# Kernel tuning notes

Hardware: AMD Instinct MI355X
Metric: run time of the kernel (lower is better)

The kernel has to match this reference:

```python
import jax, jax.numpy as jnp
import numpy as np

D1 = 512
D2 = 1024  # = 2*D1 (concat of x1,y1 along channels)
B, S = 4, 2048


def _self_attn(x, Wq, bq, Wk, bk, Wv, bv):
    # Linear layers use torch convention: out = x @ W.T + b
    q = jnp.einsum('bsd,ed->bse', x, Wq) + bq
    k = jnp.einsum('bsd,ed->bse', x, Wk) + bk
    v = jnp.einsum('bsd,ed->bse', x, Wv) + bv
    # NOTE: original module has no 1/sqrt(d) scaling — keep it faithful.
    scores = jnp.einsum('bqe,bke->bqk', q, k)  # [B,S,S]
    attn = jax.nn.softmax(scores, axis=-1)
    return jnp.einsum('bqk,bke->bqe', attn, v)


def setup_inputs() -> dict:
    key = jax.random.key(0)
    ks = jax.random.split(key, 18)
    s1 = 1.0 / np.sqrt(D1)
    s2 = 1.0 / np.sqrt(D2)
    return {
        'x': jax.random.normal(ks[0], (B, S, D1), jnp.float32),
        'y': jax.random.normal(ks[1], (B, S, D1), jnp.float32),
        'sa1_Wq': jax.random.normal(ks[2], (D1, D1), jnp.float32) * s1,
        'sa1_bq': jnp.zeros((D1,), jnp.float32),
        'sa1_Wk': jax.random.normal(ks[3], (D1, D1), jnp.float32) * s1,
        'sa1_bk': jnp.zeros((D1,), jnp.float32),
        'sa1_Wv': jax.random.normal(ks[4], (D1, D1), jnp.float32) * s1,
        'sa1_bv': jnp.zeros((D1,), jnp.float32),
        'sa2_Wq': jax.random.normal(ks[5], (D2, D2), jnp.float32) * s2,
        'sa2_bq': jnp.zeros((D2,), jnp.float32),
        'sa2_Wk': jax.random.normal(ks[6], (D2, D2), jnp.float32) * s2,
        'sa2_bk': jnp.zeros((D2,), jnp.float32),
        'sa2_Wv': jax.random.normal(ks[7], (D2, D2), jnp.float32) * s2,
        'sa2_bv': jnp.zeros((D2,), jnp.float32),
        'weight1': jnp.ones((1,), jnp.float32),
        'weight2': jnp.ones((1,), jnp.float32),
    }


def reference(x, y, sa1_Wq, sa1_bq, sa1_Wk, sa1_bk, sa1_Wv, sa1_bv,
              sa2_Wq, sa2_bq, sa2_Wk, sa2_bk, sa2_Wv, sa2_bv,
              weight1, weight2):
    x1 = _self_attn(x, sa1_Wq, sa1_bq, sa1_Wk, sa1_bk, sa1_Wv, sa1_bv)
    x1 = x1 + y * weight2
    y1 = _self_attn(y, sa1_Wq, sa1_bq, sa1_Wk, sa1_bk, sa1_Wv, sa1_bv)
    y1 = y1 + x * weight1
    temp = jnp.concatenate((x1, y1), axis=2)  # [B,S,2*D1]
    return _self_attn(temp, sa2_Wq, sa2_bq, sa2_Wk, sa2_bk, sa2_Wv, sa2_bv)
```

## Files before the change

kernel.cpp:

```cpp
#include <hip/hip_runtime.h>
#include <hip/hip_bf16.h>
#include <cstdint>
#include <cstddef>


typedef __bf16 bf16;
typedef __attribute__((ext_vector_type(8))) __bf16 bf16x8;
typedef __attribute__((ext_vector_type(4))) __bf16 bf16x4;
typedef __attribute__((ext_vector_type(4))) float f32x4;

__device__ __forceinline__ void gld16(const bf16* g, bf16* s) {
    __builtin_amdgcn_global_load_lds(
        (const __attribute__((address_space(1))) void*)g,
        (__attribute__((address_space(3))) void*)s, 16, 0, 0);
}

#define WAIT_VM8   __builtin_amdgcn_s_waitcnt(8 | (7 << 4) | (0xF << 8))
#define WAIT_VM0   __builtin_amdgcn_s_waitcnt(0 | (7 << 4) | (0xF << 8))
#define WAIT_LGKM0 __builtin_amdgcn_s_waitcnt(0xF | (7 << 4) | (0 << 8) | (3 << 14))

__device__ __forceinline__ int swz(int row, int g) {
    return row * 64 + ((g ^ (row & 7)) << 3);
}

__global__ __launch_bounds__(256) void gemm_split(
    const bf16* __restrict__ A, long lda, long psA, long bsA,
    const bf16* __restrict__ B, long ldb, long psB, long bsB,
    void* __restrict__ C, long ldc, long psC, long bsC, int mode,
    const float* __restrict__ bias, const float* __restrict__ bias2, int nsplit,
    const float* __restrict__ resid, long ldr, long bsR,
    const float* __restrict__ scale,
    int K, int split, int nx, int ny, int nz)
{
    __shared__ __align__(16) bf16 As[2][128 * 64];
    __shared__ __align__(16) bf16 Bs[2][128 * 64];

    const int t    = threadIdx.x;
    const int wave = t >> 6;
    const int lane = t & 63;
    const int wr   = wave >> 1;
    const int wc   = wave & 1;
    const int r16  = lane & 15;
    const int quad = lane >> 4;

    const int g    = blockIdx.x;
    const int xcd  = g & 7;
    const int tk   = g >> 3;
    const int nst8 = gridDim.x >> 7;
    const int st   = xcd * nst8 + (tk >> 4);
    const int p    = tk & 15;
    const int snx  = nx >> 2, sny = ny >> 2;
    const int spz  = snx * sny;
    const int zz   = st / spz;
    const int rS   = st - zz * spz;
    const int sy   = rS / snx;
    const int sx   = rS - sy * snx;
    const int yb   = sy * 4 + (p >> 2);
    const int xb   = sx * 4 + (p & 3);

    const int  kh   = zz / nz;
    const long z    = zz - (long)kh * nz;
    const long kOff = (long)kh * K;

    const long row0 = (long)yb * 128;
    const long col0 = (long)xb * 128;

    const int srow = (lane >> 3);
    const int scol = ((lane & 7) ^ srow) * 8;

    const int ktiles = K >> 6;
    const int T = split * ktiles;

    const bf16* Az = A + z * bsA;
    const bf16* Bz = B + z * bsB;

    auto prefetch = [&](int ti, int buf) {
        const int ph = ti / ktiles;
        const int kt = (ti - ph * ktiles) << 6;
        const bf16* Ab = Az + (ph == 1 ? psA : 0);
        const bf16* Bb = Bz + (ph == 2 ? psB : 0);
#pragma unroll
        for (int p2 = 0; p2 < 4; ++p2) {
            const int chunk = wave * 32 + p2 * 8;
            gld16(Ab + (row0 + chunk + srow) * lda + kt + kOff + scol, &As[buf][chunk * 64]);
            gld16(Bb + (col0 + chunk + srow) * ldb + kt + kOff + scol, &Bs[buf][chunk * 64]);
        }
    };

    f32x4 acc[4][4];
#pragma unroll
    for (int r = 0; r < 4; ++r)
#pragma unroll
        for (int c = 0; c < 4; ++c)
            acc[r][c] = (f32x4){0.f, 0.f, 0.f, 0.f};

    prefetch(0, 0);
    prefetch(1, 1);
    for (int ti = 0; ti < T; ++ti) {
        const int cur = ti & 1;
        if (ti + 1 < T) WAIT_VM8; else WAIT_VM0;
        __builtin_amdgcn_s_barrier();
        bf16x8 af[2][4], bg[2][4];
#pragma unroll
        for (int kk = 0; kk < 2; ++kk) {
            const int g0 = (kk << 2) + quad;
#pragma unroll
            for (int r = 0; r < 4; ++r)
                af[kk][r] = *reinterpret_cast<const bf16x8*>(&As[cur][swz(wr * 64 + r * 16 + r16, g0)]);
#pragma unroll
            for (int c = 0; c < 4; ++c)
                bg[kk][c] = *reinterpret_cast<const bf16x8*>(&Bs[cur][swz(wc * 64 + c * 16 + r16, g0)]);
        }
        WAIT_LGKM0;
        __builtin_amdgcn_s_barrier();
        if (ti + 2 < T) prefetch(ti + 2, cur);
#pragma unroll
        for (int kk = 0; kk < 2; ++kk)
#pragma unroll
            for (int r = 0; r < 4; ++r)
#pragma unroll
                for (int c = 0; c < 4; ++c)
                    acc[r][c] = __builtin_amdgcn_mfma_f32_16x16x32_bf16(af[kk][r], bg[kk][c], acc[r][c], 0, 0, 0);
    }

    const float scv = resid ? *scale : 0.f;

#pragma unroll
    for (int r = 0; r < 4; ++r) {
#pragma unroll
        for (int c = 0; c < 4; ++c) {
            long gcol = col0 + wc * 64 + c * 16 + r16;
            float bv = 0.f;
            if (bias) bv = (gcol < nsplit) ? bias[gcol] : bias2[gcol - nsplit];
#pragma unroll
            for (int i = 0; i < 4; ++i) {
                long grow = row0 + wr * 64 + r * 16 + quad * 4 + i;
                float val = acc[r][c][i] + bv;
                if (mode == 0) {
                    if (resid) val += resid[z * bsR + grow * ldr + gcol] * scv;
                    ((float*)C)[z * bsC + grow * ldc + gcol] = val;
                } else if (mode == 1) {
                    if (resid) val += resid[z * bsR + grow * ldr + gcol] * scv;
                    bf16* Cb = (bf16*)C + z * bsC;
                    bf16 h = (bf16)val;
                    Cb[grow * ldc + gcol] = h;
                    Cb[psC + grow * ldc + gcol] = (bf16)(val - (float)h);
                } else if (mode == 3) {
                    ((float*)C)[(long)kh * psC + z * bsC + grow * ldc + gcol] = val;
                } else {
                    long b = grow >> 11, s = grow & 2047;
                    bf16* Cb = (bf16*)C + b * bsC;
                    bf16 h = (bf16)val;
                    Cb[gcol * ldc + s] = h;
                    Cb[psC + gcol * ldc + s] = (bf16)(val - (float)h);
                }
            }
        }
    }
}

__global__ __launch_bounds__(512) void gemm256(
    const bf16* __restrict__ A, long lda, long psA, long bsA,
    const bf16* __restrict__ B, long ldb, long psB, long bsB,
    void* __restrict__ C, long ldc, long psC, long bsC, int mode,
    const float* __restrict__ bias, const float* __restrict__ bias2, int nsplit,
    int K, int split, int nx, int ny)
{
    __shared__ __align__(16) bf16 As[2][256 * 64];
    __shared__ __align__(16) bf16 Bs[2][256 * 64];

    const int t    = threadIdx.x;
    const int wave = t >> 6;
    const int lane = t & 63;
    const int wm   = wave >> 2;
    const int wn   = wave & 3;
    const int r16  = lane & 15;
    const int quad = lane >> 4;

    const int g     = blockIdx.x;
    const int chunk = gridDim.x >> 3;
    const int idx   = (g & 7) * chunk + (g >> 3);
    const int tpz   = nx * ny;
    const int z     = idx / tpz;
    const int r0i   = idx - z * tpz;
    const int ty    = r0i / nx;
    const int tx    = r0i - ty * nx;
    const long row0 = (long)ty * 256;
    const long col0 = (long)tx * 256;

    const int srow = lane >> 3;
    const int scol = ((lane & 7) ^ srow) * 8;

    const int ktiles = K >> 6;
    const int T = split * ktiles;

    const bf16* Az = A + (long)z * bsA;
    const bf16* Bz = B + (long)z * bsB;

    auto prefetch = [&](int ti, int buf) {
        const int ph = ti / ktiles;
        const int kt = (ti - ph * ktiles) << 6;
        const bf16* Ab = Az + (ph == 1 ? psA : 0);
        const bf16* Bb = Bz + (ph == 2 ? psB : 0);
#pragma unroll
        for (int p2 = 0; p2 < 4; ++p2) {
            const int chnk = wave * 32 + p2 * 8;
            gld16(Ab + (row0 + chnk + srow) * lda + kt + scol, &As[buf][chnk * 64]);
            gld16(Bb + (col0 + chnk + srow) * ldb + kt + scol, &Bs[buf][chnk * 64]);
        }
    };

    f32x4 acc[8][4];
#pragma unroll
    for (int r = 0; r < 8; ++r)
#pragma unroll
        for (int c = 0; c < 4; ++c)
            acc[r][c] = (f32x4){0.f, 0.f, 0.f, 0.f};

    prefetch(0, 0);
    prefetch(1, 1);
    for (int ti = 0; ti < T; ++ti) {
        const int cur = ti & 1;
        if (ti + 1 < T) WAIT_VM8; else WAIT_VM0;
        __builtin_amdgcn_s_barrier();

        bf16x8 afA[4][2], afB[4][2], bg[2][2][2];
#pragma unroll
        for (int kk = 0; kk < 2; ++kk) {
            const int g0 = (kk << 2) + quad;
#pragma unroll
            for (int r = 0; r < 4; ++r)
                afA[r][kk] = *reinterpret_cast<const bf16x8*>(
                    &As[cur][swz(wm * 128 + r * 16 + r16, g0)]);
        }
#pragma unroll
        for (int kk = 0; kk < 2; ++kk) {
            const int g0 = (kk << 2) + quad;
#pragma unroll
            for (int c = 0; c < 2; ++c)
                bg[0][c][kk] = *reinterpret_cast<const bf16x8*>(
                    &Bs[cur][swz(wn * 64 + c * 16 + r16, g0)]);
        }
#pragma unroll
        for (int kk = 0; kk < 2; ++kk) {
            const int g0 = (kk << 2) + quad;
#pragma unroll
            for (int c = 0; c < 2; ++c)
                bg[1][c][kk] = *reinterpret_cast<const bf16x8*>(
                    &Bs[cur][swz(wn * 64 + (2 + c) * 16 + r16, g0)]);
        }
#pragma unroll
        for (int kk = 0; kk < 2; ++kk) {
            const int g0 = (kk << 2) + quad;
#pragma unroll
            for (int r = 0; r < 4; ++r)
                afB[r][kk] = *reinterpret_cast<const bf16x8*>(
                    &As[cur][swz(wm * 128 + (4 + r) * 16 + r16, g0)]);
        }

        __builtin_amdgcn_s_setprio(1);
#pragma unroll
        for (int kk = 0; kk < 2; ++kk)
#pragma unroll
            for (int r = 0; r < 4; ++r)
#pragma unroll
                for (int c = 0; c < 2; ++c)
                    acc[r][c] = __builtin_amdgcn_mfma_f32_16x16x32_bf16(
                        afA[r][kk], bg[0][c][kk], acc[r][c], 0, 0, 0);
#pragma unroll
        for (int kk = 0; kk < 2; ++kk)
#pragma unroll
            for (int r = 0; r < 4; ++r)
#pragma unroll
                for (int c = 0; c < 2; ++c)
                    acc[r][2 + c] = __builtin_amdgcn_mfma_f32_16x16x32_bf16(
                        afA[r][kk], bg[1][c][kk], acc[r][2 + c], 0, 0, 0);
        __builtin_amdgcn_s_setprio(0);

        __builtin_amdgcn_sched_barrier(0);
        WAIT_LGKM0;
        __builtin_amdgcn_s_barrier();
        if (ti + 2 < T) prefetch(ti + 2, cur);

        __builtin_amdgcn_s_setprio(1);
#pragma unroll
        for (int kk = 0; kk < 2; ++kk)
#pragma unroll
            for (int r = 0; r < 4; ++r)
#pragma unroll
                for (int c = 0; c < 2; ++c)
                    acc[4 + r][c] = __builtin_amdgcn_mfma_f32_16x16x32_bf16(
                        afB[r][kk], bg[0][c][kk], acc[4 + r][c], 0, 0, 0);
#pragma unroll
        for (int kk = 0; kk < 2; ++kk)
#pragma unroll
            for (int r = 0; r < 4; ++r)
#pragma unroll
                for (int c = 0; c < 2; ++c)
                    acc[4 + r][2 + c] = __builtin_amdgcn_mfma_f32_16x16x32_bf16(
                        afB[r][kk], bg[1][c][kk], acc[4 + r][2 + c], 0, 0, 0);
        __builtin_amdgcn_s_setprio(0);
    }

#pragma unroll
    for (int r = 0; r < 8; ++r) {
#pragma unroll
        for (int c = 0; c < 4; ++c) {
            const long gcol = col0 + wn * 64 + c * 16 + r16;
            float bv = 0.f;
            if (bias) bv = (gcol < nsplit) ? bias[gcol] : bias2[gcol - nsplit];
#pragma unroll
            for (int i = 0; i < 4; ++i) {
                const long grow = row0 + wm * 128 + r * 16 + quad * 4 + i;
                float val = acc[r][c][i] + bv;
                if (mode == 0) {
                    ((float*)C)[(long)z * bsC + grow * ldc + gcol] = val;
                } else {
                    bf16* Cb = (bf16*)C + (long)z * bsC;
                    bf16 h = (bf16)val;
                    Cb[grow * ldc + gcol] = h;
                    Cb[psC + grow * ldc + gcol] = (bf16)(val - (float)h);
                }
            }
        }
    }
}

__global__ __launch_bounds__(256) void reduce_pv(
    const float* __restrict__ p0, const float* __restrict__ p1,
    const float* __restrict__ resid, const float* __restrict__ scale,
    bf16* __restrict__ outp, long psC)
{
    const long gid = (long)blockIdx.x * 256 + threadIdx.x;
    const long f4  = gid * 4;
    const long z   = f4 >> 20;
    const long rem = f4 & ((1L << 20) - 1);
    const long row = rem >> 9;
    const long col = rem & 511;
    const float scv = *scale;
    f32x4 a = *reinterpret_cast<const f32x4*>(p0 + f4);
    f32x4 b = *reinterpret_cast<const f32x4*>(p1 + f4);
    f32x4 r = *reinterpret_cast<const f32x4*>(resid + f4);
    bf16x4 h, l;
#pragma unroll
    for (int j = 0; j < 4; ++j) {
        float v = a[j] + b[j] + r[j] * scv;
        h[j] = (bf16)v;
        l[j] = (bf16)(v - (float)h[j]);
    }
    bf16* dst = outp + z * (2048L * 1024) + row * 1024 + col;
    *reinterpret_cast<bf16x4*>(dst) = h;
    *reinterpret_cast<bf16x4*>(dst + psC) = l;
}

__global__ __launch_bounds__(256) void softmax_planes(float* __restrict__ S)
{
    __shared__ float redm[4], reds[4];
    float* srow = S + (long)blockIdx.x * 2048;
    const int t = threadIdx.x;
    const int lane = t & 63;
    const int wave = t >> 6;

    f32x4 v0 = *reinterpret_cast<const f32x4*>(srow + t * 4);
    f32x4 v1 = *reinterpret_cast<const f32x4*>(srow + 1024 + t * 4);

    float m = v0[0];
#pragma unroll
    for (int i = 1; i < 4; ++i) m = fmaxf(m, v0[i]);
#pragma unroll
    for (int i = 0; i < 4; ++i) m = fmaxf(m, v1[i]);
#pragma unroll
    for (int off = 32; off > 0; off >>= 1) m = fmaxf(m, __shfl_xor(m, off));
    if (lane == 0) redm[wave] = m;
    __syncthreads();
    m = fmaxf(fmaxf(redm[0], redm[1]), fmaxf(redm[2], redm[3]));

    float s = 0.f;
#pragma unroll
    for (int i = 0; i < 4; ++i) { v0[i] = __expf(v0[i] - m); s += v0[i]; }
#pragma unroll
    for (int i = 0; i < 4; ++i) { v1[i] = __expf(v1[i] - m); s += v1[i]; }
#pragma unroll
    for (int off = 32; off > 0; off >>= 1) s += __shfl_xor(s, off);
    if (lane == 0) reds[wave] = s;
    __syncthreads();
    s = reds[0] + reds[1] + reds[2] + reds[3];
    float inv = 1.f / s;

    bf16x4 h0, h1, l0, l1;
#pragma unroll
    for (int i = 0; i < 4; ++i) {
        float a = v0[i] * inv, b = v1[i] * inv;
        h0[i] = (bf16)a; l0[i] = (bf16)(a - (float)h0[i]);
        h1[i] = (bf16)b; l1[i] = (bf16)(b - (float)h1[i]);
    }
    bf16* ph = (bf16*)srow;
    *reinterpret_cast<bf16x4*>(ph + t * 4) = h0;
    *reinterpret_cast<bf16x4*>(ph + 1024 + t * 4) = h1;
    *reinterpret_cast<bf16x4*>(ph + 2048 + t * 4) = l0;
    *reinterpret_cast<bf16x4*>(ph + 3072 + t * 4) = l1;
}

__global__ __launch_bounds__(256) void split2_f32(
    const float* __restrict__ in, bf16* __restrict__ hi, bf16* __restrict__ lo)
{
    long i = ((long)blockIdx.x * 256 + threadIdx.x) * 4;
    f32x4 v = *reinterpret_cast<const f32x4*>(in + i);
    bf16x4 h, l;
#pragma unroll
    for (int j = 0; j < 4; ++j) {
        h[j] = (bf16)v[j];
        l[j] = (bf16)(v[j] - (float)h[j]);
    }
    *reinterpret_cast<bf16x4*>(hi + i) = h;
    *reinterpret_cast<bf16x4*>(lo + i) = l;
}

extern "C" void kernel_launch(void* const* d_in, const int* in_sizes, int n_in,
                              void* d_out, int out_size, void* d_ws, size_t ws_size,
                              hipStream_t stream)
{
    const float* x   = (const float*)d_in[0];
    const float* y   = (const float*)d_in[1];
    const float* Wq1 = (const float*)d_in[2];
    const float* bq1 = (const float*)d_in[3];
    const float* Wk1 = (const float*)d_in[4];
    const float* bk1 = (const float*)d_in[5];
    const float* Wv1 = (const float*)d_in[6];
    const float* bv1 = (const float*)d_in[7];
    const float* Wq2 = (const float*)d_in[8];
    const float* bq2 = (const float*)d_in[9];
    const float* Wk2 = (const float*)d_in[10];
    const float* bk2 = (const float*)d_in[11];
    const float* Wv2 = (const float*)d_in[12];
    const float* bv2 = (const float*)d_in[13];
    const float* w1  = (const float*)d_in[14];
    const float* w2  = (const float*)d_in[15];
    float* out = (float*)d_out;

    const size_t MB = 1ull << 20;
    char* ws = (char*)d_ws;
    const long S = 2048, M4 = 8192, E1 = 512, E2 = 1024;
    const long W1ps = E1 * E1, W2ps = E2 * E2;

    const int cfg = (ws_size >= 207 * MB) ? 2 : 0;

    auto gemm = [&](const bf16* A, long lda, long psA, long bsA,
                    const bf16* B, long ldb, long psB, long bsB,
                    void* C, long ldc, long psC, long bsC, int mode,
                    const float* bias, const float* bias2, int nsplit,
                    const float* resid, long ldr, long bsR,
                    const float* scale, int M, int N, int K, int split,
                    int gz, int nz) {
        int nx = N / 128, ny = M / 128;
        dim3 g((unsigned)(nx * ny * gz));
        gemm_split<<<g, dim3(256), 0, stream>>>(
            A, lda, psA, bsA, B, ldb, psB, bsB, C, ldc, psC, bsC, mode,
            bias, bias2, nsplit, resid, ldr, bsR, scale, K, split, nx, ny, nz);
    };
    auto g256 = [&](const bf16* A, long lda, long psA, long bsA,
                    const bf16* B, long ldb, long psB, long bsB,
                    void* C, long ldc, long psC, long bsC, int mode,
                    const float* bias, const float* bias2, int nsplit,
                    int K, int split, int M, int N, int gz) {
        int nx = N / 256, ny = M / 256;
        gemm256<<<dim3((unsigned)(nx * ny * gz)), dim3(512), 0, stream>>>(
            A, lda, psA, bsA, B, ldb, psB, bsB, C, ldc, psC, bsC, mode,
            bias, bias2, nsplit, K, split, nx, ny);
    };
    auto conv2 = [&](const float* in, bf16* hi, bf16* lo, long n) {
        split2_f32<<<dim3((unsigned)(n / 1024)), dim3(256), 0, stream>>>(in, hi, lo);
    };

    if (cfg == 2) {
        bf16* xyp   = (bf16*)d_out;
        bf16* Wqk1p = (bf16*)(ws + 0 * MB);
        bf16* Wv1p  = (bf16*)(ws + 2 * MB);
        bf16* Wqk2p = (bf16*)(ws + 3 * MB);
        bf16* Wv2p  = (bf16*)(ws + 11 * MB);
        bf16* temp  = (bf16*)(ws + 15 * MB);
        bf16* qk    = (bf16*)(ws + 47 * MB);
        bf16* vt    = (bf16*)(ws + 111 * MB);
        float* Sc   = (float*)(ws + 143 * MB);

        const long PXY = 16384L * 512;
        const long PW1 = 1024L * 512;
        const long PW2 = 2048L * 1024;
        const long PQ1 = 16384L * 1024;
        const long PQ2 = 8192L * 2048;
        const long PT  = 8192L * 1024;
        const long BV1 = 2 * E1 * S;
        const long BV2 = 2 * E2 * S;
        const long PVH = 4L * 2048 * 512;
        float* pvScr = (float*)d_out;

        conv2(x, xyp, xyp + PXY, M4 * E1);
        conv2(y, xyp + M4 * E1, xyp + PXY + M4 * E1, M4 * E1);
        conv2(Wq1, Wqk1p, Wqk1p + PW1, W1ps);
        conv2(Wk1, Wqk1p + W1ps, Wqk1p + PW1 + W1ps, W1ps);
        conv2(Wv1, Wv1p, Wv1p + W1ps, W1ps);
        conv2(Wq2, Wqk2p, Wqk2p + PW2, W2ps);
        conv2(Wk2, Wqk2p + W2ps, Wqk2p + PW2 + W2ps, W2ps);
        conv2(Wv2, Wv2p, Wv2p + W2ps, W2ps);

        g256(xyp, E1, PXY, 0, Wqk1p, E1, PW1, 0,
             qk, 1024, PQ1, 0, 1, bq1, bk1, 512,
             512, 3, 16384, 1024, 1);
        gemm(xyp, E1, PXY, 0, Wv1p, E1, W1ps, 0,
             vt, S, E1 * S, BV1, 2, bv1, nullptr, 512,
             nullptr, 0, 0, nullptr, 16384, 512, 512, 3, 1, 1);

        g256(qk, 1024, PQ1, S * 1024, qk + 512, 1024, PQ1, S * 1024,
             Sc, S, 0, S * S, 0, nullptr, nullptr, 0, 512, 3, 2048, 2048, 4);
        softmax_planes<<<dim3(8192), dim3(256), 0, stream>>>(Sc);
        gemm((const bf16*)Sc, 4096, 2048, S * 4096, vt, S, E1 * S, BV1,
             pvScr, 512, PVH, 2048L * 512, 3, nullptr, nullptr, 0,
             nullptr, 0, 0, nullptr, 2048, 512, 1024, 3, 8, 4);
        reduce_pv<<<dim3(4096), dim3(256), 0, stream>>>(
            pvScr, pvScr + PVH, y, w2, temp, PT);

        g256(qk + M4 * 1024, 1024, PQ1, S * 1024,
             qk + M4 * 1024 + 512, 1024, PQ1, S * 1024,
             Sc, S, 0, S * S, 0, nullptr, nullptr, 0, 512, 3, 2048, 2048, 4);
        softmax_planes<<<dim3(8192), dim3(256), 0, stream>>>(Sc);
        gemm((const bf16*)Sc, 4096, 2048, S * 4096, vt + 4 * BV1, S, E1 * S, BV1,
             pvScr, 512, PVH, 2048L * 512, 3, nullptr, nullptr, 0,
             nullptr, 0, 0, nullptr, 2048, 512, 1024, 3, 8, 4);
        reduce_pv<<<dim3(4096), dim3(256), 0, stream>>>(
            pvScr, pvScr + PVH, x, w1, temp + 512, PT);

        g256(temp, E2, PT, 0, Wqk2p, E2, PW2, 0,
             qk, 2048, PQ2, 0, 1, bq2, bk2, 1024,
             1024, 3, 8192, 2048, 1);
        gemm(temp, E2, PT, 0, Wv2p, E2, W2ps, 0,
             vt, S, E2 * S, BV2, 2, bv2, nullptr, 1024,
             nullptr, 0, 0, nullptr, 8192, 1024, 1024, 1, 1, 1);
        g256(qk, 2048, PQ2, S * 2048, qk + 1024, 2048, PQ2, S * 2048,
             Sc, S, 0, S * S, 0, nullptr, nullptr, 0, 1024, 3, 2048, 2048, 4);
        softmax_planes<<<dim3(8192), dim3(256), 0, stream>>>(Sc);
        gemm((const bf16*)Sc, 4096, 2048, S * 4096, vt, S, E2 * S, BV2,
             out, E2, 0, S * E2, 0, nullptr, nullptr, 1024,
             nullptr, 0, 0, nullptr, 2048, 1024, 2048, 1, 4, 4);
    } else {
        bf16* xp = (bf16*)d_out;
        bf16* yp = xp + 2 * M4 * E1;
        bf16* Wq1p = (bf16*)(ws + 0 * MB);
        bf16* Wk1p = (bf16*)(ws + 1 * MB);
        bf16* Wv1p = (bf16*)(ws + 2 * MB);
        bf16* temp = (bf16*)(ws + 3 * MB);
        bf16* qb   = (bf16*)(ws + 35 * MB);
        bf16* kb   = (bf16*)(ws + 43 * MB);
        bf16* vt   = (bf16*)(ws + 51 * MB);
        float* Sc  = (float*)(ws + 59 * MB);
        bf16* Wq2p = (bf16*)d_out;
        bf16* Wk2p = Wq2p + 2 * W2ps;
        bf16* Wv2p = Wk2p + 2 * W2ps;

        conv2(x, xp, xp + M4 * E1, M4 * E1);
        conv2(y, yp, yp + M4 * E1, M4 * E1);
        conv2(Wq1, Wq1p, Wq1p + W1ps, W1ps);
        conv2(Wk1, Wk1p, Wk1p + W1ps, W1ps);
        conv2(Wv1, Wv1p, Wv1p + W1ps, W1ps);

        auto stage1 = [&](const bf16* sp, const float* resid, const float* scale, long colOff) {
            for (int b = 0; b < 4; ++b) {
                const bf16* sb = sp + (long)b * S * E1;
                gemm(sb, E1, M4 * E1, 0, Wq1p, E1, W1ps, 0, qb, E1, S * E1, 0, 1,
                     bq1, nullptr, 512, nullptr, 0, 0, nullptr, 2048, 512, 512, 3, 1, 1);
                gemm(sb, E1, M4 * E1, 0, Wk1p, E1, W1ps, 0, kb, E1, S * E1, 0, 1,
                     bk1, nullptr, 512, nullptr, 0, 0, nullptr, 2048, 512, 512, 3, 1, 1);
                gemm(sb, E1, M4 * E1, 0, Wv1p, E1, W1ps, 0, vt, S, E1 * S, 0, 2,
                     bv1, nullptr, 512, nullptr, 0, 0, nullptr, 2048, 512, 512, 3, 1, 1);
                gemm(qb, E1, S * E1, 0, kb, E1, S * E1, 0, Sc, S, 0, 0, 0,
                     nullptr, nullptr, 2048, nullptr, 0, 0, nullptr, 2048, 2048, 512, 3, 1, 1);
                softmax_planes<<<dim3(2048), dim3(256), 0, stream>>>(Sc);
                gemm((const bf16*)Sc, 4096, 2048, 0, vt, S, E1 * S, 0,
                     temp + colOff + (long)b * S * 1024, 1024, M4 * 1024, 0, 1,
                     nullptr, nullptr, 512, resid + (long)b * S * E1, E1, 0, scale,
                     2048, 512, 2048, 3, 1, 1);
            }
        };

        stage1(xp, y, w2, 0);
        stage1(yp, x, w1, 512);

        conv2(Wq2, Wq2p, Wq2p + W2ps, W2ps);
        conv2(Wk2, Wk2p, Wk2p + W2ps, W2ps);
        conv2(Wv2, Wv2p, Wv2p + W2ps, W2ps);

        for (int b = 0; b < 4; ++b) {
            const bf16* tb = temp + (long)b * S * E2;
            gemm(tb, E2, M4 * E2, 0, Wq2p, E2, W2ps, 0, qb, E2, S * E2, 0, 1,
                 bq2, nullptr, 1024, nullptr, 0, 0, nullptr, 2048, 1024, 1024, 3, 1, 1);
            gemm(tb, E2, M4 * E2, 0, Wk2p, E2, W2ps, 0, kb, E2, S * E2, 0, 1,
                 bk2, nullptr, 1024, nullptr, 0, 0, nullptr, 2048, 1024, 1024, 3, 1, 1);
            gemm(tb, E2, M4 * E2, 0, Wv2p, E2, W2ps, 0, vt, S, E2 * S, 0, 2,
                 bv2, nullptr, 1024, nullptr, 0, 0, nullptr, 2048, 1024, 1024, 1, 1, 1);
            gemm(qb, E2, S * E2, 0, kb, E2, S * E2, 0, Sc, S, 0, 0, 0,
                 nullptr, nullptr, 2048, nullptr, 0, 0, nullptr, 2048, 2048, 1024, 3, 1, 1);
            softmax_planes<<<dim3(2048), dim3(256), 0, stream>>>(Sc);
            gemm((const bf16*)Sc, 4096, 2048, 0, vt, S, E2 * S, 0,
                 out + (long)b * S * E2, E2, 0, 0, 0, nullptr, nullptr, 1024,
                 nullptr, 0, 0, nullptr, 2048, 1024, 2048, 1, 1, 1);
        }
    }

    (void)in_sizes; (void)n_in; (void)out_size;
}
```

Baseline: 821.9 us.

## Software-pipeline LDS fragment reads across k-halves in GEMM main loop

Restructures the GEMM inner loop so fragment reads from LDS are split by k-half (kk) instead of by row half. The next half's fragments are read while the current half's MFMAs are issued, and the first half of the next tile is read before the second-half MFMAs. This hides LDS read latency behind matrix work. The cost is more live registers (two full fragment sets) and an extra barrier per iteration, which may reduce occupancy or add sync stalls.

```diff
diff --git a/kernel.cpp b/kernel.cpp
--- a/kernel.cpp
+++ b/kernel.cpp
@@ -217,88 +217,68 @@
         for (int c = 0; c < 4; ++c)
             acc[r][c] = (f32x4){0.f, 0.f, 0.f, 0.f};
 
+    bf16x8 fA0[8], fB0[4], fA1[8], fB1[4];
+
+    auto rdset0 = [&](int cur, int kk) {
+        const int g0 = (kk << 2) + quad;
+#pragma unroll
+        for (int r = 0; r < 8; ++r)
+            fA0[r] = *reinterpret_cast<const bf16x8*>(
+                &As[cur][swz(wm * 128 + r * 16 + r16, g0)]);
+#pragma unroll
+        for (int c = 0; c < 4; ++c)
+            fB0[c] = *reinterpret_cast<const bf16x8*>(
+                &Bs[cur][swz(wn * 64 + c * 16 + r16, g0)]);
+    };
+    auto rdset1 = [&](int cur, int kk) {
+        const int g0 = (kk << 2) + quad;
+#pragma unroll
+        for (int r = 0; r < 8; ++r)
+            fA1[r] = *reinterpret_cast<const bf16x8*>(
+                &As[cur][swz(wm * 128 + r * 16 + r16, g0)]);
+#pragma unroll
+        for (int c = 0; c < 4; ++c)
+            fB1[c] = *reinterpret_cast<const bf16x8*>(
+                &Bs[cur][swz(wn * 64 + c * 16 + r16, g0)]);
+    };
+
     prefetch(0, 0);
     prefetch(1, 1);
+    WAIT_VM8;
+    __builtin_amdgcn_s_barrier();
+    rdset0(0, 0);
+
     for (int ti = 0; ti < T; ++ti) {
         const int cur = ti & 1;
-        if (ti + 1 < T) WAIT_VM8; else WAIT_VM0;
-        __builtin_amdgcn_s_barrier();
-
-        bf16x8 afA[4][2], afB[4][2], bg[2][2][2];
-#pragma unroll
-        for (int kk = 0; kk < 2; ++kk) {
-            const int g0 = (kk << 2) + quad;
-#pragma unroll
-            for (int r = 0; r < 4; ++r)
-                afA[r][kk] = *reinterpret_cast<const bf16x8*>(
-                    &As[cur][swz(wm * 128 + r * 16 + r16, g0)]);
-        }
-#pragma unroll
-        for (int kk = 0; kk < 2; ++kk) {
-            const int g0 = (kk << 2) + quad;
-#pragma unroll
-            for (int c = 0; c < 2; ++c)
-                bg[0][c][kk] = *reinterpret_cast<const bf16x8*>(
-                    &Bs[cur][swz(wn * 64 + c * 16 + r16, g0)]);
-        }
-#pragma unroll
-        for (int kk = 0; kk < 2; ++kk) {
-            const int g0 = (kk << 2) + quad;
-#pragma unroll
-            for (int c = 0; c < 2; ++c)
-                bg[1][c][kk] = *reinterpret_cast<const bf16x8*>(
-                    &Bs[cur][swz(wn * 64 + (2 + c) * 16 + r16, g0)]);
-        }
-#pragma unroll
-        for (int kk = 0; kk < 2; ++kk) {
-            const int g0 = (kk << 2) + quad;
-#pragma unroll
-            for (int r = 0; r < 4; ++r)
-                afB[r][kk] = *reinterpret_cast<const bf16x8*>(
-                    &As[cur][swz(wm * 128 + (4 + r) * 16 + r16, g0)]);
-        }
-
+
+        rdset1(cur, 1);
+        __builtin_amdgcn_sched_barrier(0);
         __builtin_amdgcn_s_setprio(1);
 #pragma unroll
-        for (int kk = 0; kk < 2; ++kk)
-#pragma unroll
-            for (int r = 0; r < 4; ++r)
-#pragma unroll
-                for (int c = 0; c < 2; ++c)
-                    acc[r][c] = __builtin_amdgcn_mfma_f32_16x16x32_bf16(
-                        afA[r][kk], bg[0][c][kk], acc[r][c], 0, 0, 0);
-#pragma unroll
-        for (int kk = 0; kk < 2; ++kk)
-#pragma unroll
-            for (int r = 0; r < 4; ++r)
-#pragma unroll
-                for (int c = 0; c < 2; ++c)
-                    acc[r][2 + c] = __builtin_amdgcn_mfma_f32_16x16x32_bf16(
-                        afA[r][kk], bg[1][c][kk], acc[r][2 + c], 0, 0, 0);
+        for (int r = 0; r < 8; ++r)
+#pragma unroll
+            for (int c = 0; c < 4; ++c)
+                acc[r][c] = __builtin_amdgcn_mfma_f32_16x16x32_bf16(
+                    fA0[r], fB0[c], acc[r][c], 0, 0, 0);
         __builtin_amdgcn_s_setprio(0);
-
         __builtin_amdgcn_sched_barrier(0);
+
         WAIT_LGKM0;
         __builtin_amdgcn_s_barrier();
         if (ti + 2 < T) prefetch(ti + 2, cur);
-
+        if (ti + 1 < T) {
+            if (ti + 2 < T) WAIT_VM8; else WAIT_VM0;
+            __builtin_amdgcn_s_barrier();
+            rdset0(cur ^ 1, 0);
+        }
+        __builtin_amdgcn_sched_barrier(0);
         __builtin_amdgcn_s_setprio(1);
 #pragma unroll
-        for (int kk = 0; kk < 2; ++kk)
-#pragma unroll
-            for (int r = 0; r < 4; ++r)
-#pragma unroll
-                for (int c = 0; c < 2; ++c)
-                    acc[4 + r][c] = __builtin_amdgcn_mfma_f32_16x16x32_bf16(
-                        afB[r][kk], bg[0][c][kk], acc[4 + r][c], 0, 0, 0);
-#pragma unroll
-        for (int kk = 0; kk < 2; ++kk)
-#pragma unroll
-            for (int r = 0; r < 4; ++r)
-#pragma unroll
-                for (int c = 0; c < 2; ++c)
-                    acc[4 + r][2 + c] = __builtin_amdgcn_mfma_f32_16x16x32_bf16(
-                        afB[r][kk], bg[1][c][kk], acc[4 + r][2 + c], 0, 0, 0);
+        for (int r = 0; r < 8; ++r)
+#pragma unroll
+            for (int c = 0; c < 4; ++c)
+                acc[r][c] = __builtin_amdgcn_mfma_f32_16x16x32_bf16(
+                    fA1[r], fB1[c], acc[r][c], 0, 0, 0);
         __builtin_amdgcn_s_setprio(0);
     }
 
```

Result: slower. 880.6 us (+7.2%).
